# Performance work log

Hardware: AMD Instinct MI355X
Metric: run time of the kernel (lower is better)

Reference implementation:

```python
import jax, jax.numpy as jnp
import numpy as np

G = 4096        # graphs
NPG = 32        # nodes per graph
N = G * NPG     # total nodes
D = 256         # hidden (inv node feat) dim
SH = 256        # shared / node-MLP hidden dim
HDG = 50        # graph head dim
HDN = 3         # node head dim
NB = 2          # num branches (dataset IDs)


def setup_inputs() -> dict:
    key = jax.random.key(0)
    ks = jax.random.split(key, 8)
    s = 0.02
    return {
        "x": jax.random.normal(ks[0], (N, D), jnp.float32),
        "dataset_name": jax.random.randint(ks[1], (G,), 0, NB, jnp.int32),
        "batch": (jnp.arange(N) // NPG).astype(jnp.int32),
        "Wgs": jax.random.normal(ks[2], (NB, D, SH), jnp.float32) * s,
        "bgs": jnp.zeros((NB, SH), jnp.float32),
        "Wgh": jax.random.normal(ks[3], (NB, SH, 2 * HDG), jnp.float32) * s,
        "bgh": jnp.zeros((NB, 2 * HDG), jnp.float32),
        "Wn1": jax.random.normal(ks[4], (NB, D, SH), jnp.float32) * s,
        "bn1": jnp.zeros((NB, SH), jnp.float32),
        "Wn2": jax.random.normal(ks[5], (NB, SH, 2 * HDN), jnp.float32) * s,
        "bn2": jnp.zeros((NB, 2 * HDN), jnp.float32),
    }


def reference(x, dataset_name, batch, Wgs, bgs, Wgh, bgh, Wn1, bn1, Wn2, bn2):
    n_nodes = x.shape[0]
    n_graphs = dataset_name.shape[0]

    # ---- graph pooling (mean) : scatter-reduce nodes -> graphs ----
    counts = jax.ops.segment_sum(jnp.ones((n_nodes,), x.dtype), batch, num_segments=n_graphs)
    x_graph = jax.ops.segment_sum(x, batch, num_segments=n_graphs) / counts[:, None]  # [G, D]

    # ---- graph head: per-branch shared MLP + head, then branch dispatch ----
    hg = jax.nn.relu(jnp.einsum("gd,bds->bgs", x_graph, Wgs) + bgs[:, None, :])       # [B, G, SH]
    og = jnp.einsum("bgs,bsh->bgh", hg, Wgh) + bgh[:, None, :]                        # [B, G, 2*HDG]
    out_g = og[dataset_name, jnp.arange(n_graphs)]                                    # [G, 2*HDG]
    g_head = out_g[:, :HDG]
    g_var = out_g[:, HDG:] ** 2

    # ---- node head (mlp type): per-branch MLP on nodes, dispatch by node's graph ID ----
    node_branch = dataset_name[batch]                                                 # [N]
    hn = jax.nn.relu(jnp.einsum("nd,bds->bns", x, Wn1) + bn1[:, None, :])             # [B, N, SH]
    on = jnp.einsum("bns,bsh->bnh", hn, Wn2) + bn2[:, None, :]                        # [B, N, 2*HDN]
    out_n = on[node_branch, jnp.arange(n_nodes)]                                      # [N, 2*HDN]
    n_head = out_n[:, :HDN]
    n_var = out_n[:, HDN:] ** 2

    # (outputs, outputs_var) flattened: heads then variance heads
    return (g_head, n_head, g_var, n_var)
```

## Files before the change

### kernel.cpp

```cpp
#include <hip/hip_runtime.h>
#include <hip/hip_bf16.h>


#define G_   4096
#define NPG_ 32
#define NN_  (G_*NPG_)
#define D_   256
#define SH_  256
#define HDG_ 50
#define HDN_ 3

#define OFF_GH 0
#define OFF_NH (G_*HDG_)
#define OFF_GV (OFF_NH + NN_*HDN_)
#define OFF_NV (OFF_GV + G_*HDG_)

typedef short v8s __attribute__((ext_vector_type(8)));
typedef short v4s __attribute__((ext_vector_type(4)));
typedef float v4f __attribute__((ext_vector_type(4)));

__device__ __forceinline__ float bfu2f(unsigned short u) {
    return __uint_as_float(((unsigned int)u) << 16);
}
__device__ __forceinline__ unsigned short f2bfu(float v) {
    __hip_bfloat16 b = __float2bfloat16(v);
    return *reinterpret_cast<unsigned short*>(&b);
}

#define MFMA16(a, b, c) __builtin_amdgcn_mfma_f32_16x16x32_bf16((a), (b), (c), 0, 0, 0)

__global__ __launch_bounds__(256) void wpack(const float* __restrict__ Wn1,
                                             const float* __restrict__ Wgs,
                                             const float* __restrict__ Wgh,
                                             const float* __restrict__ Wn2,
                                             unsigned short* __restrict__ out) {
    const int idx = blockIdx.x * 256 + threadIdx.x;
    float v;
    if (idx < 131072) {
        const int b = idx >> 16, rem = idx & 65535, s = rem >> 8, d = rem & 255;
        v = Wn1[b * 65536 + d * 256 + s];
    } else if (idx < 262144) {
        const int i2 = idx - 131072;
        const int np = i2 >> 8, d = i2 & 255;
        v = Wgs[(np >> 8) * 65536 + d * 256 + (np & 255)];
    } else if (idx < 327680) {
        const int i3 = idx - 262144;
        const int npp = i3 >> 8, k = i3 & 255;
        const int b = npp >> 7, c = npp & 127;
        v = (c < 100) ? Wgh[b * 25600 + k * 100 + c] : 0.f;
    } else {
        const int i4 = idx - 327680;
        const int b = i4 >> 12, rem = i4 & 4095, n = rem >> 8, k = rem & 255;
        v = (n < 6) ? Wn2[b * 1536 + k * 6 + n] : 0.f;
    }
    out[idx] = f2bfu(v);
}

__global__ __launch_bounds__(256) void prep_node(const float* __restrict__ x,
                                                 const int* __restrict__ dsname,
                                                 const unsigned short* __restrict__ Wn1T,
                                                 const float* __restrict__ bn1,
                                                 const unsigned short* __restrict__ Wn2b,
                                                 const float* __restrict__ bn2,
                                                 unsigned short* __restrict__ xg,
                                                 float* __restrict__ out) {
    __shared__ __align__(16) unsigned short xs[NPG_ * 264];
    __shared__ __align__(16) float red[4 * 256];
    const int g = blockIdx.x, t = threadIdx.x;
    const int wave = t >> 6, lane = t & 63;
    const int l15 = lane & 15, quad = lane >> 4;
    const int b = dsname[g];

    const int colb = (t & 63) * 4;
    const int rb = t >> 6;
    float s0 = 0.f, s1 = 0.f, s2 = 0.f, s3 = 0.f;
    #pragma unroll
    for (int k = 0; k < 8; k++) {
        const int row = rb + k * 4;
        const float4 v = *(const float4*)(x + (size_t)g * 8192 + row * 256 + colb);
        s0 += v.x; s1 += v.y; s2 += v.z; s3 += v.w;
        v4s bv; bv[0] = (short)f2bfu(v.x); bv[1] = (short)f2bfu(v.y);
                bv[2] = (short)f2bfu(v.z); bv[3] = (short)f2bfu(v.w);
        *(v4s*)(&xs[row * 264 + colb]) = bv;
    }
    *(float4*)(&red[rb * 256 + colb]) = make_float4(s0, s1, s2, s3);
    __syncthreads();

    xg[(size_t)g * 256 + t] =
        f2bfu((red[t] + red[256 + t] + red[512 + t] + red[768 + t]) * (1.0f / NPG_));

    v4f acc[2][4];
    #pragma unroll
    for (int mt = 0; mt < 2; mt++)
        #pragma unroll
        for (int nt = 0; nt < 4; nt++) acc[mt][nt] = (v4f){0.f, 0.f, 0.f, 0.f};

    const unsigned short* Ab = &xs[l15 * 264 + quad * 8];
    const unsigned short* Bb = Wn1T + b * 65536 + (wave * 64 + l15) * 256 + quad * 8;

    #pragma unroll
    for (int kt = 0; kt < 8; kt++) {
        const int ko = kt * 32;
        v8s a0 = *(const v8s*)(Ab + ko);
        v8s a1 = *(const v8s*)(Ab + 16 * 264 + ko);
        v8s b0 = *(const v8s*)(Bb + ko);
        v8s b1 = *(const v8s*)(Bb + 4096 + ko);
        v8s b2 = *(const v8s*)(Bb + 8192 + ko);
        v8s b3 = *(const v8s*)(Bb + 12288 + ko);
        acc[0][0] = MFMA16(a0, b0, acc[0][0]);
        acc[1][0] = MFMA16(a1, b0, acc[1][0]);
        acc[0][1] = MFMA16(a0, b1, acc[0][1]);
        acc[1][1] = MFMA16(a1, b1, acc[1][1]);
        acc[0][2] = MFMA16(a0, b2, acc[0][2]);
        acc[1][2] = MFMA16(a1, b2, acc[1][2]);
        acc[0][3] = MFMA16(a0, b3, acc[0][3]);
        acc[1][3] = MFMA16(a1, b3, acc[1][3]);
    }
    __syncthreads();

    #pragma unroll
    for (int nt = 0; nt < 4; nt++) {
        const int col = wave * 64 + nt * 16 + l15;
        const float bias = bn1[b * 256 + col];
        #pragma unroll
        for (int mt = 0; mt < 2; mt++)
            #pragma unroll
            for (int r = 0; r < 4; r++) {
                const int row = mt * 16 + quad * 4 + r;
                const float v = acc[mt][nt][r] + bias;
                xs[row * 264 + col] = f2bfu(v > 0.f ? v : 0.f);
            }
    }
    __syncthreads();

    {
        const int mt = wave & 1, kh = wave >> 1;
        v4f a2 = (v4f){0.f, 0.f, 0.f, 0.f};
        const unsigned short* Bp = Wn2b + b * 4096 + l15 * 256 + quad * 8;
        #pragma unroll
        for (int j = 0; j < 4; j++) {
            const int ko = (kh * 4 + j) * 32;
            v8s av = *(const v8s*)(&xs[(mt * 16 + l15) * 264 + ko + quad * 8]);
            v8s bv = *(const v8s*)(Bp + ko);
            a2 = MFMA16(av, bv, a2);
        }
        #pragma unroll
        for (int r = 0; r < 4; r++)
            red[kh * 512 + (mt * 16 + quad * 4 + r) * 16 + l15] = a2[r];
    }
    __syncthreads();

    if (t < NPG_ * 2 * HDN_) {
        const int i = t / 6, c = t % 6;
        const float o = red[i * 16 + c] + red[512 + i * 16 + c] + bn2[b * 6 + c];
        const int n = g * NPG_ + i;
        if (c < HDN_) out[OFF_NH + n * HDN_ + c] = o;
        else          out[OFF_NV + n * HDN_ + (c - HDN_)] = o * o;
    }
}

__global__ __launch_bounds__(256) void graph_mfma2(const unsigned short* __restrict__ xg,
                                                   const int* __restrict__ dsname,
                                                   const unsigned short* __restrict__ WgsT,
                                                   const float* __restrict__ bgs,
                                                   const unsigned short* __restrict__ WghP,
                                                   const float* __restrict__ bgh,
                                                   float* __restrict__ out) {
    __shared__ __align__(16) unsigned short xs[32 * 264];
    __shared__ int bls[32];
    const int gbase = blockIdx.x * 32;
    const int t = threadIdx.x;
    const int wave = t >> 6, lane = t & 63;
    const int l15 = lane & 15, quad = lane >> 4;
    if (t < 32) bls[t] = dsname[gbase + t];

    #pragma unroll
    for (int k = 0; k < 4; k++) {
        const int flat = k * 2048 + t * 8;
        *(v8s*)(&xs[(flat >> 8) * 264 + (flat & 255)]) =
            *(const v8s*)(xg + (size_t)gbase * 256 + flat);
    }
    __syncthreads();

    v4f acc[2][8];
    #pragma unroll
    for (int mt = 0; mt < 2; mt++)
        #pragma unroll
        for (int nt = 0; nt < 8; nt++) acc[mt][nt] = (v4f){0.f, 0.f, 0.f, 0.f};

    const unsigned short* Ab = &xs[l15 * 264 + quad * 8];
    const unsigned short* Bb = WgsT + (wave * 128 + l15) * 256 + quad * 8;

    #pragma unroll
    for (int kt = 0; kt < 8; kt++) {
        const int ko = kt * 32;
        v8s a0 = *(const v8s*)(Ab + ko);
        v8s a1 = *(const v8s*)(Ab + 16 * 264 + ko);
        #pragma unroll
        for (int nt = 0; nt < 8; nt++) {
            v8s bv = *(const v8s*)(Bb + nt * 16 * 256 + ko);
            acc[0][nt] = MFMA16(a0, bv, acc[0][nt]);
            acc[1][nt] = MFMA16(a1, bv, acc[1][nt]);
        }
    }
    __syncthreads();

    {
        const int bw = wave >> 1;
        #pragma unroll
        for (int nt = 0; nt < 8; nt++) {
            const int sp = wave * 128 + nt * 16 + l15;
            const int s_local = sp & 255;
            const float bias = bgs[sp];
            #pragma unroll
            for (int mt = 0; mt < 2; mt++)
                #pragma unroll
                for (int r = 0; r < 4; r++) {
                    const int row = mt * 16 + quad * 4 + r;
                    if (bls[row] == bw) {
                        const float v = acc[mt][nt][r] + bias;
                        xs[row * 264 + s_local] = f2bfu(v > 0.f ? v : 0.f);
                    }
                }
        }
    }
    __syncthreads();

    v4f acc2[2][4];
    #pragma unroll
    for (int mt = 0; mt < 2; mt++)
        #pragma unroll
        for (int nt = 0; nt < 4; nt++) acc2[mt][nt] = (v4f){0.f, 0.f, 0.f, 0.f};

    const unsigned short* B2 = WghP + ((wave * 4) * 16 + l15) * 256 + quad * 8;
    #pragma unroll
    for (int kt = 0; kt < 8; kt++) {
        const int ko = kt * 32;
        v8s a0 = *(const v8s*)(&xs[l15 * 264 + ko + quad * 8]);
        v8s a1 = *(const v8s*)(&xs[(16 + l15) * 264 + ko + quad * 8]);
        #pragma unroll
        for (int nt = 0; nt < 4; nt++) {
            v8s bv = *(const v8s*)(B2 + nt * 16 * 256 + ko);
            acc2[0][nt] = MFMA16(a0, bv, acc2[0][nt]);
            acc2[1][nt] = MFMA16(a1, bv, acc2[1][nt]);
        }
    }

    #pragma unroll
    for (int nt = 0; nt < 4; nt++) {
        const int npp  = (wave * 4 + nt) * 16 + l15;
        const int bo   = npp >> 7, c = npp & 127;
        if (c < 2 * HDG_) {
            const float bias = bgh[bo * 2 * HDG_ + c];
            #pragma unroll
            for (int mt = 0; mt < 2; mt++)
                #pragma unroll
                for (int r = 0; r < 4; r++) {
                    const int row = mt * 16 + quad * 4 + r;
                    if (bls[row] == bo) {
                        const float o = acc2[mt][nt][r] + bias;
                        const int g = gbase + row;
                        if (c < HDG_) out[OFF_GH + g * HDG_ + c] = o;
                        else          out[OFF_GV + g * HDG_ + (c - HDG_)] = o * o;
                    }
                }
        }
    }
}

extern "C" void kernel_launch(void* const* d_in, const int* in_sizes, int n_in,
                              void* d_out, int out_size, void* d_ws, size_t ws_size,
                              hipStream_t stream) {
    const float* x      = (const float*)d_in[0];
    const int*   dsname = (const int*)d_in[1];
    const float* Wgs = (const float*)d_in[3];
    const float* bgs = (const float*)d_in[4];
    const float* Wgh = (const float*)d_in[5];
    const float* bgh = (const float*)d_in[6];
    const float* Wn1 = (const float*)d_in[7];
    const float* bn1 = (const float*)d_in[8];
    const float* Wn2 = (const float*)d_in[9];
    const float* bn2 = (const float*)d_in[10];
    float* out = (float*)d_out;

    unsigned short* wsbuf = (unsigned short*)d_ws;
    unsigned short* Wn1T  = wsbuf;
    unsigned short* WgsT  = wsbuf + 131072;
    unsigned short* WghP  = wsbuf + 262144;
    unsigned short* Wn2b  = wsbuf + 327680;
    unsigned short* xg    = wsbuf + 335872;

    wpack      <<<1312,    256, 0, stream>>>(Wn1, Wgs, Wgh, Wn2, wsbuf);
    prep_node  <<<G_,      256, 0, stream>>>(x, dsname, Wn1T, bn1, Wn2b, bn2, xg, out);
    graph_mfma2<<<G_ / 32, 256, 0, stream>>>(xg, dsname, WgsT, bgs, WghP, bgh, out);
}
```

Baseline: 279.5 us.

## Process two graphs per block in node MLP to reuse weight fragments

The node-MLP kernel now handles two graphs per block (64 rows). When both graphs use the same branch, each Wn1 B-fragment load feeds four M-tiles instead of two, halving weight traffic per node; otherwise it runs two separate passes. It also issues all eight x loads before converting them, and drops the final cross-wave reduction for the second layer by giving each wave the full K loop. The cost is more registers and LDS per block, a launch bound of 3 blocks per CU, and half as many blocks in the grid.

```diff
diff --git a/kernel.cpp b/kernel.cpp
--- a/kernel.cpp
+++ b/kernel.cpp
@@ -56,106 +56,154 @@
     out[idx] = f2bfu(v);
 }
 
-__global__ __launch_bounds__(256) void prep_node(const float* __restrict__ x,
-                                                 const int* __restrict__ dsname,
-                                                 const unsigned short* __restrict__ Wn1T,
-                                                 const float* __restrict__ bn1,
-                                                 const unsigned short* __restrict__ Wn2b,
-                                                 const float* __restrict__ bn2,
-                                                 unsigned short* __restrict__ xg,
-                                                 float* __restrict__ out) {
-    __shared__ __align__(16) unsigned short xs[NPG_ * 264];
-    __shared__ __align__(16) float red[4 * 256];
-    const int g = blockIdx.x, t = threadIdx.x;
+#define TSZ (NPG_ * 264)
+__global__ __launch_bounds__(256, 3) void prep_node2(const float* __restrict__ x,
+                                                     const int* __restrict__ dsname,
+                                                     const unsigned short* __restrict__ Wn1T,
+                                                     const float* __restrict__ bn1,
+                                                     const unsigned short* __restrict__ Wn2b,
+                                                     const float* __restrict__ bn2,
+                                                     unsigned short* __restrict__ xg,
+                                                     float* __restrict__ out) {
+    __shared__ __align__(16) unsigned short xs[2 * TSZ];
+    __shared__ __align__(16) float red[2 * 4 * 256];
+    __shared__ int bls[2];
+    const int g0 = blockIdx.x * 2, t = threadIdx.x;
     const int wave = t >> 6, lane = t & 63;
     const int l15 = lane & 15, quad = lane >> 4;
-    const int b = dsname[g];
+    if (t < 2) bls[t] = dsname[g0 + t];
 
     const int colb = (t & 63) * 4;
     const int rb = t >> 6;
-    float s0 = 0.f, s1 = 0.f, s2 = 0.f, s3 = 0.f;
-    #pragma unroll
-    for (int k = 0; k < 8; k++) {
-        const int row = rb + k * 4;
-        const float4 v = *(const float4*)(x + (size_t)g * 8192 + row * 256 + colb);
-        s0 += v.x; s1 += v.y; s2 += v.z; s3 += v.w;
-        v4s bv; bv[0] = (short)f2bfu(v.x); bv[1] = (short)f2bfu(v.y);
-                bv[2] = (short)f2bfu(v.z); bv[3] = (short)f2bfu(v.w);
-        *(v4s*)(&xs[row * 264 + colb]) = bv;
-    }
-    *(float4*)(&red[rb * 256 + colb]) = make_float4(s0, s1, s2, s3);
-    __syncthreads();
-
-    xg[(size_t)g * 256 + t] =
+    #pragma unroll
+    for (int j = 0; j < 2; j++) {
+        const float* xb = x + (size_t)(g0 + j) * 8192;
+        float4 v[8];
+        #pragma unroll
+        for (int k = 0; k < 8; k++)
+            v[k] = *(const float4*)(xb + (rb + k * 4) * 256 + colb);
+        float s0 = 0.f, s1 = 0.f, s2 = 0.f, s3 = 0.f;
+        #pragma unroll
+        for (int k = 0; k < 8; k++) {
+            s0 += v[k].x; s1 += v[k].y; s2 += v[k].z; s3 += v[k].w;
+            v4s bv; bv[0] = (short)f2bfu(v[k].x); bv[1] = (short)f2bfu(v[k].y);
+                    bv[2] = (short)f2bfu(v[k].z); bv[3] = (short)f2bfu(v[k].w);
+            *(v4s*)(&xs[j * TSZ + (rb + k * 4) * 264 + colb]) = bv;
+        }
+        *(float4*)(&red[(j * 4 + rb) * 256 + colb]) = make_float4(s0, s1, s2, s3);
+    }
+    __syncthreads();
+
+    xg[(size_t)g0 * 256 + t] =
         f2bfu((red[t] + red[256 + t] + red[512 + t] + red[768 + t]) * (1.0f / NPG_));
-
-    v4f acc[2][4];
-    #pragma unroll
-    for (int mt = 0; mt < 2; mt++)
+    xg[(size_t)(g0 + 1) * 256 + t] =
+        f2bfu((red[1024 + t] + red[1280 + t] + red[1536 + t] + red[1792 + t]) * (1.0f / NPG_));
+
+    const int b0 = bls[0], b1 = bls[1];
+    v4f acc[4][4];
+    #pragma unroll
+    for (int mt = 0; mt < 4; mt++)
         #pragma unroll
         for (int nt = 0; nt < 4; nt++) acc[mt][nt] = (v4f){0.f, 0.f, 0.f, 0.f};
 
-    const unsigned short* Ab = &xs[l15 * 264 + quad * 8];
-    const unsigned short* Bb = Wn1T + b * 65536 + (wave * 64 + l15) * 256 + quad * 8;
-
-    #pragma unroll
-    for (int kt = 0; kt < 8; kt++) {
-        const int ko = kt * 32;
-        v8s a0 = *(const v8s*)(Ab + ko);
-        v8s a1 = *(const v8s*)(Ab + 16 * 264 + ko);
-        v8s b0 = *(const v8s*)(Bb + ko);
-        v8s b1 = *(const v8s*)(Bb + 4096 + ko);
-        v8s b2 = *(const v8s*)(Bb + 8192 + ko);
-        v8s b3 = *(const v8s*)(Bb + 12288 + ko);
-        acc[0][0] = MFMA16(a0, b0, acc[0][0]);
-        acc[1][0] = MFMA16(a1, b0, acc[1][0]);
-        acc[0][1] = MFMA16(a0, b1, acc[0][1]);
-        acc[1][1] = MFMA16(a1, b1, acc[1][1]);
-        acc[0][2] = MFMA16(a0, b2, acc[0][2]);
-        acc[1][2] = MFMA16(a1, b2, acc[1][2]);
-        acc[0][3] = MFMA16(a0, b3, acc[0][3]);
-        acc[1][3] = MFMA16(a1, b3, acc[1][3]);
-    }
-    __syncthreads();
-
-    #pragma unroll
-    for (int nt = 0; nt < 4; nt++) {
-        const int col = wave * 64 + nt * 16 + l15;
-        const float bias = bn1[b * 256 + col];
-        #pragma unroll
-        for (int mt = 0; mt < 2; mt++)
+    const int aoff = l15 * 264 + quad * 8;
+    const unsigned short* Bb0 = Wn1T + b0 * 65536 + (wave * 64 + l15) * 256 + quad * 8;
+
+    if (b0 == b1) {
+        #pragma unroll
+        for (int kt = 0; kt < 8; kt++) {
+            const int ko = kt * 32;
+            v8s bf0 = *(const v8s*)(Bb0 + ko);
+            v8s bf1 = *(const v8s*)(Bb0 + 4096 + ko);
+            v8s bf2 = *(const v8s*)(Bb0 + 8192 + ko);
+            v8s bf3 = *(const v8s*)(Bb0 + 12288 + ko);
+            #pragma unroll
+            for (int mt = 0; mt < 4; mt++) {
+                v8s a = *(const v8s*)(&xs[(mt >> 1) * TSZ + (mt & 1) * 16 * 264 + aoff + ko]);
+                acc[mt][0] = MFMA16(a, bf0, acc[mt][0]);
+                acc[mt][1] = MFMA16(a, bf1, acc[mt][1]);
+                acc[mt][2] = MFMA16(a, bf2, acc[mt][2]);
+                acc[mt][3] = MFMA16(a, bf3, acc[mt][3]);
+            }
+        }
+    } else {
+        const unsigned short* Bb1 = Wn1T + b1 * 65536 + (wave * 64 + l15) * 256 + quad * 8;
+        #pragma unroll
+        for (int kt = 0; kt < 8; kt++) {
+            const int ko = kt * 32;
+            v8s bf0 = *(const v8s*)(Bb0 + ko);
+            v8s bf1 = *(const v8s*)(Bb0 + 4096 + ko);
+            v8s bf2 = *(const v8s*)(Bb0 + 8192 + ko);
+            v8s bf3 = *(const v8s*)(Bb0 + 12288 + ko);
+            #pragma unroll
+            for (int mt = 0; mt < 2; mt++) {
+                v8s a = *(const v8s*)(&xs[(mt & 1) * 16 * 264 + aoff + ko]);
+                acc[mt][0] = MFMA16(a, bf0, acc[mt][0]);
+                acc[mt][1] = MFMA16(a, bf1, acc[mt][1]);
+                acc[mt][2] = MFMA16(a, bf2, acc[mt][2]);
+                acc[mt][3] = MFMA16(a, bf3, acc[mt][3]);
+            }
+        }
+        #pragma unroll
+        for (int kt = 0; kt < 8; kt++) {
+            const int ko = kt * 32;
+            v8s bf0 = *(const v8s*)(Bb1 + ko);
+            v8s bf1 = *(const v8s*)(Bb1 + 4096 + ko);
+            v8s bf2 = *(const v8s*)(Bb1 + 8192 + ko);
+            v8s bf3 = *(const v8s*)(Bb1 + 12288 + ko);
+            #pragma unroll
+            for (int mt = 2; mt < 4; mt++) {
+                v8s a = *(const v8s*)(&xs[TSZ + (mt & 1) * 16 * 264 + aoff + ko]);
+                acc[mt][0] = MFMA16(a, bf0, acc[mt][0]);
+                acc[mt][1] = MFMA16(a, bf1, acc[mt][1]);
+                acc[mt][2] = MFMA16(a, bf2, acc[mt][2]);
+                acc[mt][3] = MFMA16(a, bf3, acc[mt][3]);
+            }
+        }
+    }
+    __syncthreads();
+
+    #pragma unroll
+    for (int mt = 0; mt < 4; mt++) {
+        const int j = mt >> 1;
+        const int bj = j ? b1 : b0;
+        #pragma unroll
+        for (int nt = 0; nt < 4; nt++) {
+            const int col = wave * 64 + nt * 16 + l15;
+            const float bias = bn1[bj * 256 + col];
             #pragma unroll
             for (int r = 0; r < 4; r++) {
-                const int row = mt * 16 + quad * 4 + r;
+                const int row = (mt & 1) * 16 + quad * 4 + r;
                 const float v = acc[mt][nt][r] + bias;
-                xs[row * 264 + col] = f2bfu(v > 0.f ? v : 0.f);
-            }
+                xs[j * TSZ + row * 264 + col] = f2bfu(v > 0.f ? v : 0.f);
+            }
+        }
     }
     __syncthreads();
 
     {
-        const int mt = wave & 1, kh = wave >> 1;
+        const int j = wave >> 1, mtl = wave & 1;
+        const int bj = j ? b1 : b0;
         v4f a2 = (v4f){0.f, 0.f, 0.f, 0.f};
-        const unsigned short* Bp = Wn2b + b * 4096 + l15 * 256 + quad * 8;
-        #pragma unroll
-        for (int j = 0; j < 4; j++) {
-            const int ko = (kh * 4 + j) * 32;
-            v8s av = *(const v8s*)(&xs[(mt * 16 + l15) * 264 + ko + quad * 8]);
+        const unsigned short* Bp = Wn2b + bj * 4096 + l15 * 256 + quad * 8;
+        #pragma unroll
+        for (int kt = 0; kt < 8; kt++) {
+            const int ko = kt * 32;
+            v8s av = *(const v8s*)(&xs[j * TSZ + (mtl * 16 + l15) * 264 + ko + quad * 8]);
             v8s bv = *(const v8s*)(Bp + ko);
             a2 = MFMA16(av, bv, a2);
         }
-        #pragma unroll
-        for (int r = 0; r < 4; r++)
-            red[kh * 512 + (mt * 16 + quad * 4 + r) * 16 + l15] = a2[r];
-    }
-    __syncthreads();
-
-    if (t < NPG_ * 2 * HDN_) {
-        const int i = t / 6, c = t % 6;
-        const float o = red[i * 16 + c] + red[512 + i * 16 + c] + bn2[b * 6 + c];
-        const int n = g * NPG_ + i;
-        if (c < HDN_) out[OFF_NH + n * HDN_ + c] = o;
-        else          out[OFF_NV + n * HDN_ + (c - HDN_)] = o * o;
+        if (l15 < 6) {
+            const float bias = bn2[bj * 6 + l15];
+            #pragma unroll
+            for (int r = 0; r < 4; r++) {
+                const int row = mtl * 16 + quad * 4 + r;
+                const int n = (g0 + j) * NPG_ + row;
+                const float o = a2[r] + bias;
+                if (l15 < HDN_) out[OFF_NH + n * HDN_ + l15] = o;
+                else            out[OFF_NV + n * HDN_ + (l15 - HDN_)] = o * o;
+            }
+        }
     }
 }
 
@@ -291,6 +339,6 @@
     unsigned short* xg    = wsbuf + 335872;
 
     wpack      <<<1312,    256, 0, stream>>>(Wn1, Wgs, Wgh, Wn2, wsbuf);
-    prep_node  <<<G_,      256, 0, stream>>>(x, dsname, Wn1T, bn1, Wn2b, bn2, xg, out);
+    prep_node2 <<<G_ / 2,  256, 0, stream>>>(x, dsname, Wn1T, bn1, Wn2b, bn2, xg, out);
     graph_mfma2<<<G_ / 32, 256, 0, stream>>>(xg, dsname, WgsT, bgs, WghP, bgh, out);
 }
```

Result: no change. 280.4 us (+0.3%).

## Persistent branch-bucketed node kernel with register-resident weights and prefetch

Applied to the files above, without the earlier changes.

Replaces the one-block-per-graph node MLP kernel with a persistent kernel of 256 blocks of 512 threads. A new single-block kernel first buckets graphs by branch ID. Each persistent block serves one branch and keeps its Wn1/Wn2 slices in registers, so weights are no longer reloaded from global memory for every graph. The next graph's x tile is prefetched into registers while the current one is processed. In exchange it adds an extra launch, a serial bucketing step, heavy register use, and several barriers per graph iteration, and occupancy may fall.

```diff
diff --git a/kernel.cpp b/kernel.cpp
--- a/kernel.cpp
+++ b/kernel.cpp
@@ -56,8 +56,26 @@
     out[idx] = f2bfu(v);
 }
 
-__global__ __launch_bounds__(256) void prep_node(const float* __restrict__ x,
-                                                 const int* __restrict__ dsname,
+__global__ void build_glist(const int* __restrict__ dsname,
+                            int* __restrict__ glist,
+                            int* __restrict__ gcnt) {
+    __shared__ int cnt[2];
+    const int t = threadIdx.x;
+    if (t < 2) cnt[t] = 0;
+    __syncthreads();
+    for (int i = 0; i < 16; i++) {
+        const int g = i * 256 + t;
+        const int b = dsname[g];
+        const int slot = atomicAdd(&cnt[b], 1);
+        glist[b * G_ + slot] = g;
+    }
+    __syncthreads();
+    if (t < 2) gcnt[t] = cnt[t];
+}
+
+__global__ __launch_bounds__(512) void node_pers(const float* __restrict__ x,
+                                                 const int* __restrict__ glist,
+                                                 const int* __restrict__ gcnt,
                                                  const unsigned short* __restrict__ Wn1T,
                                                  const float* __restrict__ bn1,
                                                  const unsigned short* __restrict__ Wn2b,
@@ -65,97 +83,129 @@
                                                  unsigned short* __restrict__ xg,
                                                  float* __restrict__ out) {
     __shared__ __align__(16) unsigned short xs[NPG_ * 264];
-    __shared__ __align__(16) float red[4 * 256];
-    const int g = blockIdx.x, t = threadIdx.x;
+    __shared__ __align__(16) float red[8 * 256];
+    const int t = threadIdx.x;
     const int wave = t >> 6, lane = t & 63;
     const int l15 = lane & 15, quad = lane >> 4;
-    const int b = dsname[g];
-
+    const int br = blockIdx.x & 1;
+    const int bslot = blockIdx.x >> 1;
+    const int cnt = gcnt[br];
+
+    const int base_n = (wave & 1) * 128 + (wave >> 1) * 32;
+
+    v8s B1[2][8];
+    float bias1[2];
+    #pragma unroll
+    for (int nt = 0; nt < 2; nt++) {
+        const unsigned short* bp = Wn1T + br * 65536 + (base_n + nt * 16 + l15) * 256 + quad * 8;
+        #pragma unroll
+        for (int kt = 0; kt < 8; kt++) B1[nt][kt] = *(const v8s*)(bp + kt * 32);
+        bias1[nt] = bn1[br * 256 + base_n + nt * 16 + l15];
+    }
+
+    v8s B2[4];
+    if (wave < 4) {
+        const int kh = wave >> 1;
+        const unsigned short* bp = Wn2b + br * 4096 + l15 * 256 + kh * 128 + quad * 8;
+        #pragma unroll
+        for (int j = 0; j < 4; j++) B2[j] = *(const v8s*)(bp + j * 32);
+    }
+    float bias2 = 0.f; int i2 = 0, c2 = 0;
+    if (t < 192) { i2 = t / 6; c2 = t % 6; bias2 = bn2[br * 6 + c2]; }
+
+    const int rb = t >> 6;
     const int colb = (t & 63) * 4;
-    const int rb = t >> 6;
-    float s0 = 0.f, s1 = 0.f, s2 = 0.f, s3 = 0.f;
-    #pragma unroll
-    for (int k = 0; k < 8; k++) {
-        const int row = rb + k * 4;
-        const float4 v = *(const float4*)(x + (size_t)g * 8192 + row * 256 + colb);
-        s0 += v.x; s1 += v.y; s2 += v.z; s3 += v.w;
-        v4s bv; bv[0] = (short)f2bfu(v.x); bv[1] = (short)f2bfu(v.y);
-                bv[2] = (short)f2bfu(v.z); bv[3] = (short)f2bfu(v.w);
-        *(v4s*)(&xs[row * 264 + colb]) = bv;
-    }
-    *(float4*)(&red[rb * 256 + colb]) = make_float4(s0, s1, s2, s3);
-    __syncthreads();
-
-    xg[(size_t)g * 256 + t] =
-        f2bfu((red[t] + red[256 + t] + red[512 + t] + red[768 + t]) * (1.0f / NPG_));
-
-    v4f acc[2][4];
-    #pragma unroll
-    for (int mt = 0; mt < 2; mt++)
-        #pragma unroll
-        for (int nt = 0; nt < 4; nt++) acc[mt][nt] = (v4f){0.f, 0.f, 0.f, 0.f};
-
-    const unsigned short* Ab = &xs[l15 * 264 + quad * 8];
-    const unsigned short* Bb = Wn1T + b * 65536 + (wave * 64 + l15) * 256 + quad * 8;
-
-    #pragma unroll
-    for (int kt = 0; kt < 8; kt++) {
-        const int ko = kt * 32;
-        v8s a0 = *(const v8s*)(Ab + ko);
-        v8s a1 = *(const v8s*)(Ab + 16 * 264 + ko);
-        v8s b0 = *(const v8s*)(Bb + ko);
-        v8s b1 = *(const v8s*)(Bb + 4096 + ko);
-        v8s b2 = *(const v8s*)(Bb + 8192 + ko);
-        v8s b3 = *(const v8s*)(Bb + 12288 + ko);
-        acc[0][0] = MFMA16(a0, b0, acc[0][0]);
-        acc[1][0] = MFMA16(a1, b0, acc[1][0]);
-        acc[0][1] = MFMA16(a0, b1, acc[0][1]);
-        acc[1][1] = MFMA16(a1, b1, acc[1][1]);
-        acc[0][2] = MFMA16(a0, b2, acc[0][2]);
-        acc[1][2] = MFMA16(a1, b2, acc[1][2]);
-        acc[0][3] = MFMA16(a0, b3, acc[0][3]);
-        acc[1][3] = MFMA16(a1, b3, acc[1][3]);
-    }
-    __syncthreads();
-
-    #pragma unroll
-    for (int nt = 0; nt < 4; nt++) {
-        const int col = wave * 64 + nt * 16 + l15;
-        const float bias = bn1[b * 256 + col];
+
+    int gi = bslot;
+    int g = glist[br * G_ + ((gi < cnt) ? gi : (cnt - 1))];
+    float4 pv[4];
+    #pragma unroll
+    for (int k = 0; k < 4; k++)
+        pv[k] = *(const float4*)(x + (size_t)g * 8192 + (rb * 4 + k) * 256 + colb);
+
+    for (; gi < cnt; gi += 128) {
+        const int gcur = g;
+        float s0 = 0.f, s1 = 0.f, s2 = 0.f, s3 = 0.f;
+        #pragma unroll
+        for (int k = 0; k < 4; k++) {
+            s0 += pv[k].x; s1 += pv[k].y; s2 += pv[k].z; s3 += pv[k].w;
+            v4s bv; bv[0] = (short)f2bfu(pv[k].x); bv[1] = (short)f2bfu(pv[k].y);
+                    bv[2] = (short)f2bfu(pv[k].z); bv[3] = (short)f2bfu(pv[k].w);
+            *(v4s*)(&xs[(rb * 4 + k) * 264 + colb]) = bv;
+        }
+        *(float4*)(&red[rb * 256 + colb]) = make_float4(s0, s1, s2, s3);
+
+        {
+            const int gi2 = gi + 128;
+            const int gn = glist[br * G_ + ((gi2 < cnt) ? gi2 : (cnt - 1))];
+            #pragma unroll
+            for (int k = 0; k < 4; k++)
+                pv[k] = *(const float4*)(x + (size_t)gn * 8192 + (rb * 4 + k) * 256 + colb);
+            g = gn;
+        }
+        __syncthreads();
+
+        if (t < 256) {
+            float m = 0.f;
+            #pragma unroll
+            for (int r = 0; r < 8; r++) m += red[r * 256 + t];
+            xg[(size_t)gcur * 256 + t] = f2bfu(m * (1.0f / NPG_));
+        }
+
+        v4f acc[2][2];
         #pragma unroll
         for (int mt = 0; mt < 2; mt++)
             #pragma unroll
-            for (int r = 0; r < 4; r++) {
-                const int row = mt * 16 + quad * 4 + r;
-                const float v = acc[mt][nt][r] + bias;
-                xs[row * 264 + col] = f2bfu(v > 0.f ? v : 0.f);
+            for (int nt = 0; nt < 2; nt++) acc[mt][nt] = (v4f){0.f, 0.f, 0.f, 0.f};
+        #pragma unroll
+        for (int kt = 0; kt < 8; kt++) {
+            const int ko = kt * 32;
+            v8s a0 = *(const v8s*)(&xs[l15 * 264 + quad * 8 + ko]);
+            v8s a1 = *(const v8s*)(&xs[(16 + l15) * 264 + quad * 8 + ko]);
+            #pragma unroll
+            for (int nt = 0; nt < 2; nt++) {
+                acc[0][nt] = MFMA16(a0, B1[nt][kt], acc[0][nt]);
+                acc[1][nt] = MFMA16(a1, B1[nt][kt], acc[1][nt]);
             }
-    }
-    __syncthreads();
-
-    {
-        const int mt = wave & 1, kh = wave >> 1;
-        v4f a2 = (v4f){0.f, 0.f, 0.f, 0.f};
-        const unsigned short* Bp = Wn2b + b * 4096 + l15 * 256 + quad * 8;
-        #pragma unroll
-        for (int j = 0; j < 4; j++) {
-            const int ko = (kh * 4 + j) * 32;
-            v8s av = *(const v8s*)(&xs[(mt * 16 + l15) * 264 + ko + quad * 8]);
-            v8s bv = *(const v8s*)(Bp + ko);
-            a2 = MFMA16(av, bv, a2);
-        }
-        #pragma unroll
-        for (int r = 0; r < 4; r++)
-            red[kh * 512 + (mt * 16 + quad * 4 + r) * 16 + l15] = a2[r];
-    }
-    __syncthreads();
-
-    if (t < NPG_ * 2 * HDN_) {
-        const int i = t / 6, c = t % 6;
-        const float o = red[i * 16 + c] + red[512 + i * 16 + c] + bn2[b * 6 + c];
-        const int n = g * NPG_ + i;
-        if (c < HDN_) out[OFF_NH + n * HDN_ + c] = o;
-        else          out[OFF_NV + n * HDN_ + (c - HDN_)] = o * o;
+        }
+        __syncthreads();
+
+        #pragma unroll
+        for (int nt = 0; nt < 2; nt++) {
+            const int col = base_n + nt * 16 + l15;
+            #pragma unroll
+            for (int mt = 0; mt < 2; mt++)
+                #pragma unroll
+                for (int r = 0; r < 4; r++) {
+                    const int row = mt * 16 + quad * 4 + r;
+                    const float v = acc[mt][nt][r] + bias1[nt];
+                    xs[row * 264 + col] = f2bfu(v > 0.f ? v : 0.f);
+                }
+        }
+        __syncthreads();
+
+        if (wave < 4) {
+            const int mtl = wave & 1, kh = wave >> 1;
+            v4f a2 = (v4f){0.f, 0.f, 0.f, 0.f};
+            #pragma unroll
+            for (int j = 0; j < 4; j++) {
+                const int ko = kh * 128 + j * 32;
+                v8s av = *(const v8s*)(&xs[(mtl * 16 + l15) * 264 + ko + quad * 8]);
+                a2 = MFMA16(av, B2[j], a2);
+            }
+            #pragma unroll
+            for (int r = 0; r < 4; r++)
+                red[kh * 512 + (mtl * 16 + quad * 4 + r) * 16 + l15] = a2[r];
+        }
+        __syncthreads();
+
+        if (t < 192) {
+            const float o = red[i2 * 16 + c2] + red[512 + i2 * 16 + c2] + bias2;
+            const int n = gcur * NPG_ + i2;
+            if (c2 < HDN_) out[OFF_NH + n * HDN_ + c2] = o;
+            else           out[OFF_NV + n * HDN_ + (c2 - HDN_)] = o * o;
+        }
+        __syncthreads();
     }
 }
 
@@ -289,8 +339,11 @@
     unsigned short* WghP  = wsbuf + 262144;
     unsigned short* Wn2b  = wsbuf + 327680;
     unsigned short* xg    = wsbuf + 335872;
+    int* glist = (int*)((char*)d_ws + 2768896);
+    int* gcnt  = (int*)((char*)d_ws + 2801664);
 
     wpack      <<<1312,    256, 0, stream>>>(Wn1, Wgs, Wgh, Wn2, wsbuf);
-    prep_node  <<<G_,      256, 0, stream>>>(x, dsname, Wn1T, bn1, Wn2b, bn2, xg, out);
+    build_glist<<<1,       256, 0, stream>>>(dsname, glist, gcnt);
+    node_pers  <<<256,     512, 0, stream>>>(x, glist, gcnt, Wn1T, bn1, Wn2b, bn2, xg, out);
     graph_mfma2<<<G_ / 32, 256, 0, stream>>>(xg, dsname, WgsT, bgs, WghP, bgh, out);
 }
```

Result: faster. 245.1 us (-12.3%).
